# Optimization experiments

Hardware: AMD Instinct MI355X
Metric: run time of the kernel (lower is better)

The kernel has to match this reference:

```python
import jax, jax.numpy as jnp
import numpy as np

DECAY = 0.8
EPS = 1e-05


def setup_inputs() -> dict:
    key = jax.random.key(0)
    k1, k2, k3 = jax.random.split(key, 3)
    x = jax.random.normal(k1, (8, 2048, 256), dtype=jnp.float32)
    embed = jax.random.normal(k2, (8192, 256), dtype=jnp.float32)
    cluster_size = jnp.zeros((8192,), dtype=jnp.float32)
    embed_avg = jax.random.normal(k3, (8192, 256), dtype=jnp.float32)
    return {"x": x, "embed": embed, "cluster_size": cluster_size, "embed_avg": embed_avg}


def reference(x, embed, cluster_size, embed_avg):
    codebook_size, dim = embed.shape
    shape = x.shape
    flatten = x.reshape(-1, dim)  # [N, d]

    dist = -(jnp.sum(flatten ** 2, axis=1, keepdims=True)
             - 2.0 * flatten @ embed.T
             + jnp.sum(embed ** 2, axis=1)[None, :])  # [N, C]
    embed_ind_flat = jnp.argmax(dist, axis=-1)  # [N]
    embed_ind = embed_ind_flat.reshape(shape[:-1])
    quantize = jnp.take(embed, embed_ind_flat, axis=0).reshape(shape)

    # EMA update (training branch). onehot matmuls expressed as segment sums.
    counts = jax.ops.segment_sum(jnp.ones_like(embed_ind_flat, dtype=x.dtype),
                                 embed_ind_flat, num_segments=codebook_size)  # [C]
    embed_sum = jax.ops.segment_sum(flatten, embed_ind_flat,
                                    num_segments=codebook_size)  # [C, d]
    cluster_size_new = cluster_size * DECAY + (1.0 - DECAY) * counts
    embed_avg_new = embed_avg * DECAY + (1.0 - DECAY) * embed_sum
    smoothed = (cluster_size_new + EPS) / (cluster_size_new.sum() + codebook_size * EPS)
    cs = smoothed * cluster_size_new.sum()
    embed_normalized = embed_avg_new / cs[:, None]

    return quantize, embed_ind, embed_normalized, cluster_size_new, embed_avg_new
```

## Files before the change

kernel.cpp:

```cpp
#include <hip/hip_runtime.h>
#include <hip/hip_bf16.h>

#define DECAY_F 0.8f
#define OMD_F   0.2f
#define EPS_F   1e-5f

#define NROWS 16384
#define CBOOK 8192
#define DIM   256
#define KSPLIT 768

#define WS_KEYS   0u
#define WS_ENORM  131072u
#define WS_COUNTS 163840u
#define WS_TOTAL  196608u
#define WS_XSPLIT 262144u
#define WS_ESPLIT_OFF (262144u + 25165824u)
#define WS_NEED   (WS_ESPLIT_OFF + 12582912u)

#define O_QUANT 0
#define O_IND   4194304
#define O_NORM  4210688
#define O_CSN   6307840
#define O_AVG   6316032

typedef __attribute__((ext_vector_type(8))) short short8;
typedef __attribute__((ext_vector_type(4))) float f32x4;
typedef __attribute__((ext_vector_type(4))) unsigned short us4;

__device__ __forceinline__ unsigned int fkey(float f) {
    unsigned int b = __float_as_uint(f);
    return (b & 0x80000000u) ? ~b : (b | 0x80000000u);
}
__device__ __forceinline__ unsigned short f2bf(float f) {
    unsigned int u = __float_as_uint(f);
    unsigned int r = (u + 0x7FFFu + ((u >> 16) & 1u)) >> 16;
    return (unsigned short)r;
}
__device__ __forceinline__ float bf2f(unsigned short h) {
    return __uint_as_float(((unsigned int)h) << 16);
}

#define GLOAD_LDS16(g, l) \
    __builtin_amdgcn_global_load_lds((const __attribute__((address_space(1))) void*)(g), \
                                     (__attribute__((address_space(3))) void*)(l), 16, 0, 0)

__global__ __launch_bounds__(256) void init_avg_kernel(const float* __restrict__ embed_avg,
                                                       float* __restrict__ avg_out) {
    int i = blockIdx.x * 256 + threadIdx.x;
    float4 v = ((const float4*)embed_avg)[i];
    v.x *= DECAY_F; v.y *= DECAY_F; v.z *= DECAY_F; v.w *= DECAY_F;
    ((float4*)avg_out)[i] = v;
}

__global__ __launch_bounds__(256) void xsplit_kernel(const float* __restrict__ src,
                                                     unsigned short* __restrict__ dst) {
    int i = blockIdx.x * 256 + threadIdx.x;
    int e4  = i * 4;
    int row = e4 >> 8;
    int k   = e4 & 255;
    float4 v = ((const float4*)src)[i];
    us4 hi, lo;
    hi.x = f2bf(v.x); lo.x = f2bf(v.x - bf2f(hi.x));
    hi.y = f2bf(v.y); lo.y = f2bf(v.y - bf2f(hi.y));
    hi.z = f2bf(v.z); lo.z = f2bf(v.z - bf2f(hi.z));
    hi.w = f2bf(v.w); lo.w = f2bf(v.w - bf2f(hi.w));
    unsigned short* base = dst + (size_t)row * KSPLIT + k;
    *(us4*)(base + 0)   = hi;
    *(us4*)(base + 256) = lo;
    *(us4*)(base + 512) = hi;
}

__global__ __launch_bounds__(256) void esplit_kernel(const float* __restrict__ embed,
                                                     unsigned short* __restrict__ dst,
                                                     float* __restrict__ enorm) {
    int row  = (blockIdx.x * 256 + threadIdx.x) >> 6;
    int lane = threadIdx.x & 63;
    float4 v = *(const float4*)&embed[row * DIM + lane * 4];
    float s = v.x * v.x + v.y * v.y + v.z * v.z + v.w * v.w;
    for (int m = 32; m >= 1; m >>= 1) s += __shfl_xor(s, m, 64);
    if (lane == 0) enorm[row] = s;
    us4 hi, lo;
    hi.x = f2bf(v.x); lo.x = f2bf(v.x - bf2f(hi.x));
    hi.y = f2bf(v.y); lo.y = f2bf(v.y - bf2f(hi.y));
    hi.z = f2bf(v.z); lo.z = f2bf(v.z - bf2f(hi.z));
    hi.w = f2bf(v.w); lo.w = f2bf(v.w - bf2f(hi.w));
    unsigned short* base = dst + (size_t)row * KSPLIT + lane * 4;
    *(us4*)(base + 0)   = hi;
    *(us4*)(base + 256) = hi;
    *(us4*)(base + 512) = lo;
}

__global__ __launch_bounds__(256, 4) void mfma_argmin_kernel(const unsigned short* __restrict__ A,
                                                             const unsigned short* __restrict__ B,
                                                             const float* __restrict__ enorm,
                                                             unsigned long long* __restrict__ keys) {
    __shared__ __align__(16) unsigned short Al[2][128 * 32];
    __shared__ __align__(16) unsigned short Bl[2][128 * 32];

    const int tid  = threadIdx.x;
    const int lane = tid & 63;
    const int wid  = tid >> 6;
    const int wr = wid >> 1, wc = wid & 1;
    const int mBase = blockIdx.y * 128;
    const int nBase = blockIdx.x * 128;

    const int lr = lane & 15;
    const int hk = lane >> 4;

    f32x4 acc[4][4];
#pragma unroll
    for (int i = 0; i < 4; i++)
#pragma unroll
        for (int n = 0; n < 4; n++) acc[i][n] = (f32x4)0.f;

    const int r0 = tid >> 2;
    const int ck = (((tid & 3) ^ ((r0 >> 1) & 3)) << 3);
    const unsigned short* gA0 = A + (size_t)(mBase + r0) * KSPLIT + ck;
    const unsigned short* gA1 = gA0 + (size_t)64 * KSPLIT;
    const unsigned short* gB0 = B + (size_t)(nBase + r0) * KSPLIT + ck;
    const unsigned short* gB1 = gB0 + (size_t)64 * KSPLIT;

#define STAGE(b, kk) do { \
    GLOAD_LDS16(gA0 + (kk), &Al[b][tid * 8]); \
    GLOAD_LDS16(gA1 + (kk), &Al[b][(tid + 256) * 8]); \
    GLOAD_LDS16(gB0 + (kk), &Bl[b][tid * 8]); \
    GLOAD_LDS16(gB1 + (kk), &Bl[b][(tid + 256) * 8]); \
} while (0)

    const int co = ((hk ^ ((lr >> 1) & 3)) << 3);
    int aoff[4], boff[4];
#pragma unroll
    for (int i = 0; i < 4; i++) {
        aoff[i] = (wr * 64 + i * 16 + lr) * 32 + co;
        boff[i] = (wc * 64 + i * 16 + lr) * 32 + co;
    }

    STAGE(0, 0);
    __syncthreads();

#pragma unroll 2
    for (int t = 0; t < 24; ++t) {
        const int cur = t & 1;
        if (t < 23) STAGE(cur ^ 1, (t + 1) * 32);

        short8 af[4], bf4[4];
#pragma unroll
        for (int i = 0; i < 4; i++) af[i]  = *(const short8*)&Al[cur][aoff[i]];
#pragma unroll
        for (int n = 0; n < 4; n++) bf4[n] = *(const short8*)&Bl[cur][boff[n]];
#pragma unroll
        for (int i = 0; i < 4; i++)
#pragma unroll
            for (int n = 0; n < 4; n++)
                acc[i][n] = __builtin_amdgcn_mfma_f32_16x16x32_bf16(af[i], bf4[n], acc[i][n], 0, 0, 0);

        __syncthreads();
    }
#undef STAGE

    float en4[4];
    int   c4[4];
#pragma unroll
    for (int n = 0; n < 4; n++) {
        c4[n]  = nBase + wc * 64 + n * 16 + lr;
        en4[n] = enorm[c4[n]];
    }
#pragma unroll
    for (int i = 0; i < 4; i++) {
#pragma unroll
        for (int reg = 0; reg < 4; reg++) {
            float bs = 3.4e38f; int bc = 0;
#pragma unroll
            for (int n = 0; n < 4; n++) {
                float s = en4[n] - 2.f * acc[i][n][reg];
                if (s < bs || (s == bs && c4[n] < bc)) { bs = s; bc = c4[n]; }
            }
            unsigned long long key =
                ((unsigned long long)fkey(bs) << 32) | (unsigned int)bc;
#pragma unroll
            for (int m = 8; m >= 1; m >>= 1) {
                unsigned long long o = __shfl_xor(key, m, 64);
                if (o < key) key = o;
            }
            if (lr == 0)
                atomicMin(&keys[mBase + wr * 64 + i * 16 + hk * 4 + reg], key);
        }
    }
}

#define BM 64
#define BN 256
#define KB 16
#define NSPLIT 4

__global__ __launch_bounds__(256) void argmin_kernel(const float* __restrict__ x,
                                                     const float* __restrict__ embed,
                                                     const float* __restrict__ enorm,
                                                     unsigned long long* __restrict__ keys) {
    __shared__ float xs[KB][BM];
    __shared__ float es[KB][BN];

    const int tid = threadIdx.x;
    const int tx = tid & 31;
    const int ty = tid >> 5;
    const int rowBase = blockIdx.x * BM;
    const int cStart = blockIdx.y * (CBOOK / NSPLIT);

    float bestS[8];
    int   bestC[8];
#pragma unroll
    for (int i = 0; i < 8; i++) { bestS[i] = 3.4e38f; bestC[i] = 0; }

    float acc[8][8];

    for (int cb = 0; cb < CBOOK / NSPLIT; cb += BN) {
        const int cbase = cStart + cb;
#pragma unroll
        for (int i = 0; i < 8; i++)
#pragma unroll
            for (int j = 0; j < 8; j++) acc[i][j] = 0.f;

        for (int kk = 0; kk < DIM; kk += KB) {
            __syncthreads();
            {
                int r  = tid >> 2;
                int k4 = (tid & 3) * 4;
                float4 v = *(const float4*)&x[(rowBase + r) * DIM + kk + k4];
                xs[k4 + 0][r] = v.x; xs[k4 + 1][r] = v.y;
                xs[k4 + 2][r] = v.z; xs[k4 + 3][r] = v.w;
            }
            {
                const float4* src = (const float4*)&embed[(cbase + tid) * DIM + kk];
#pragma unroll
                for (int q = 0; q < 4; q++) {
                    float4 v = src[q];
                    es[q * 4 + 0][tid] = v.x; es[q * 4 + 1][tid] = v.y;
                    es[q * 4 + 2][tid] = v.z; es[q * 4 + 3][tid] = v.w;
                }
            }
            __syncthreads();
#pragma unroll
            for (int k = 0; k < KB; k++) {
                float xr[8], er[8];
                *(float4*)&xr[0] = *(const float4*)&xs[k][ty * 8];
                *(float4*)&xr[4] = *(const float4*)&xs[k][ty * 8 + 4];
                *(float4*)&er[0] = *(const float4*)&es[k][tx * 4];
                *(float4*)&er[4] = *(const float4*)&es[k][128 + tx * 4];
#pragma unroll
                for (int i = 0; i < 8; i++)
#pragma unroll
                    for (int j = 0; j < 8; j++)
                        acc[i][j] = fmaf(xr[i], er[j], acc[i][j]);
            }
        }
#pragma unroll
        for (int j = 0; j < 8; j++) {
            int c = cbase + ((j < 4) ? (tx * 4 + j) : (128 + tx * 4 + (j - 4)));
            float en = enorm[c];
#pragma unroll
            for (int i = 0; i < 8; i++) {
                float s = en - 2.f * acc[i][j];
                if (s < bestS[i]) { bestS[i] = s; bestC[i] = c; }
            }
        }
    }

#pragma unroll
    for (int i = 0; i < 8; i++) {
        unsigned long long key =
            ((unsigned long long)fkey(bestS[i]) << 32) | (unsigned int)bestC[i];
        for (int m = 16; m >= 1; m >>= 1) {
            unsigned long long o = __shfl_xor(key, m, 64);
            if (o < key) key = o;
        }
        if (tx == 0) atomicMin(&keys[rowBase + ty * 8 + i], key);
    }
}

__global__ __launch_bounds__(256) void scatter_kernel(const float* __restrict__ x,
                                                      const float* __restrict__ embed,
                                                      const unsigned long long* __restrict__ keys,
                                                      float* __restrict__ quant,
                                                      float* __restrict__ ind_out,
                                                      float* __restrict__ counts,
                                                      float* __restrict__ avg_out) {
    int i = blockIdx.x * 256 + threadIdx.x;
    int row = i >> 6;
    int c4  = (i & 63) * 4;
    int idx = (int)(keys[row] & 0xFFFFFFFFull);
    float4 e = *(const float4*)&embed[idx * DIM + c4];
    *(float4*)&quant[row * DIM + c4] = e;
    float4 xv = *(const float4*)&x[row * DIM + c4];
    atomicAdd(&avg_out[idx * DIM + c4 + 0], OMD_F * xv.x);
    atomicAdd(&avg_out[idx * DIM + c4 + 1], OMD_F * xv.y);
    atomicAdd(&avg_out[idx * DIM + c4 + 2], OMD_F * xv.z);
    atomicAdd(&avg_out[idx * DIM + c4 + 3], OMD_F * xv.w);
    if ((i & 63) == 0) {
        ind_out[row] = (float)idx;
        atomicAdd(&counts[idx], 1.0f);
    }
}

__global__ __launch_bounds__(256) void csn_kernel(const float* __restrict__ cluster_size,
                                                  const float* __restrict__ counts,
                                                  float* __restrict__ csn_out,
                                                  float* __restrict__ total) {
    int c = blockIdx.x * 256 + threadIdx.x;
    float v = DECAY_F * cluster_size[c] + OMD_F * counts[c];
    csn_out[c] = v;
    float s = v;
    for (int m = 32; m >= 1; m >>= 1) s += __shfl_xor(s, m, 64);
    __shared__ float ws4[4];
    if ((threadIdx.x & 63) == 0) ws4[threadIdx.x >> 6] = s;
    __syncthreads();
    if (threadIdx.x == 0) atomicAdd(total, ws4[0] + ws4[1] + ws4[2] + ws4[3]);
}

__global__ __launch_bounds__(256) void norm_kernel(const float* __restrict__ avg_new,
                                                   const float* __restrict__ csn,
                                                   const float* __restrict__ total,
                                                   float* __restrict__ out) {
    int i = blockIdx.x * 256 + threadIdx.x;
    int c = i >> 6;
    float tot = *total;
    float smoothed = (csn[c] + EPS_F) / (tot + (float)CBOOK * EPS_F);
    float cs = smoothed * tot;
    float4 v = ((const float4*)avg_new)[i];
    v.x = v.x / cs; v.y = v.y / cs; v.z = v.z / cs; v.w = v.w / cs;
    ((float4*)out)[i] = v;
}

extern "C" void kernel_launch(void* const* d_in, const int* in_sizes, int n_in,
                              void* d_out, int out_size, void* d_ws, size_t ws_size,
                              hipStream_t stream) {
    const float* x            = (const float*)d_in[0];
    const float* embed        = (const float*)d_in[1];
    const float* cluster_size = (const float*)d_in[2];
    const float* embed_avg    = (const float*)d_in[3];
    float* out = (float*)d_out;
    char*  ws  = (char*)d_ws;

    unsigned long long* keys = (unsigned long long*)(ws + WS_KEYS);
    float* enorm  = (float*)(ws + WS_ENORM);
    float* counts = (float*)(ws + WS_COUNTS);
    float* total  = (float*)(ws + WS_TOTAL);

    hipMemsetAsync(ws + WS_KEYS, 0xFF, NROWS * 8, stream);
    hipMemsetAsync(ws + WS_COUNTS, 0, CBOOK * 4 + 4, stream);

    init_avg_kernel<<<(CBOOK * DIM / 4) / 256, 256, 0, stream>>>(embed_avg, out + O_AVG);

    if (ws_size >= (size_t)WS_NEED) {
        unsigned short* xsplit = (unsigned short*)(ws + WS_XSPLIT);
        unsigned short* esplit = (unsigned short*)(ws + WS_ESPLIT_OFF);
        xsplit_kernel<<<(NROWS * DIM / 4) / 256, 256, 0, stream>>>(x, xsplit);
        esplit_kernel<<<CBOOK / 4, 256, 0, stream>>>(embed, esplit, enorm);
        dim3 grid(CBOOK / 128, NROWS / 128);
        mfma_argmin_kernel<<<grid, 256, 0, stream>>>(xsplit, esplit, enorm, keys);
    } else {
        esplit_kernel<<<CBOOK / 4, 256, 0, stream>>>(embed, (unsigned short*)(ws + WS_XSPLIT), enorm);
        dim3 grid(NROWS / BM, NSPLIT);
        argmin_kernel<<<grid, 256, 0, stream>>>(x, embed, enorm, keys);
    }

    scatter_kernel<<<(NROWS * DIM / 4) / 256, 256, 0, stream>>>(
        x, embed, keys, out + O_QUANT, out + O_IND, counts, out + O_AVG);

    csn_kernel<<<CBOOK / 256, 256, 0, stream>>>(cluster_size, counts, out + O_CSN, total);

    norm_kernel<<<(CBOOK * DIM / 4) / 256, 256, 0, stream>>>(
        out + O_AVG, out + O_CSN, total, out + O_NORM);
}
```

Baseline: 404.8 us.

## Rewrite split-bf16 distance GEMM with 32x32 MFMA, 256x128 tiles, triple buffering

Replaces the 128x128-tile, 16x16x32 MFMA distance kernel with a 256x128 tile using 32x32x16 bf16 MFMA, three-stage LDS buffering with explicit vmcnt waits and a single barrier per step, and a swizzled 1D block order for L2 locality. The larger tile and bigger MFMA shape raise arithmetic intensity and cut LDS reads per flop, and deeper prefetch hides global latency. In exchange, register and LDS use rise (occupancy hint drops to 2 blocks per SIMD set), and the hand-written waitcnt logic must match the number of outstanding loads exactly.

```diff
diff --git a/kernel.cpp b/kernel.cpp
--- a/kernel.cpp
+++ b/kernel.cpp
@@ -24,9 +24,10 @@
 #define O_CSN   6307840
 #define O_AVG   6316032
 
-typedef __attribute__((ext_vector_type(8))) short short8;
-typedef __attribute__((ext_vector_type(4))) float f32x4;
-typedef __attribute__((ext_vector_type(4))) unsigned short us4;
+typedef __attribute__((ext_vector_type(8)))  short short8;
+typedef __attribute__((ext_vector_type(4)))  float f32x4;
+typedef __attribute__((ext_vector_type(16))) float f32x16;
+typedef __attribute__((ext_vector_type(4)))  unsigned short us4;
 
 __device__ __forceinline__ unsigned int fkey(float f) {
     unsigned int b = __float_as_uint(f);
@@ -91,100 +92,138 @@
     *(us4*)(base + 512) = lo;
 }
 
-__global__ __launch_bounds__(256, 4) void mfma_argmin_kernel(const unsigned short* __restrict__ A,
-                                                             const unsigned short* __restrict__ B,
-                                                             const float* __restrict__ enorm,
-                                                             unsigned long long* __restrict__ keys) {
-    __shared__ __align__(16) unsigned short Al[2][128 * 32];
-    __shared__ __align__(16) unsigned short Bl[2][128 * 32];
+__global__ __launch_bounds__(256, 2) void mfma32_argmin_kernel(
+        const unsigned short* __restrict__ A,
+        const unsigned short* __restrict__ B,
+        const float* __restrict__ enorm,
+        unsigned long long* __restrict__ keys) {
+    __shared__ __align__(16) unsigned short Al[3][8192];
+    __shared__ __align__(16) unsigned short Bl[3][4096];
 
     const int tid  = threadIdx.x;
     const int lane = tid & 63;
     const int wid  = tid >> 6;
-    const int wr = wid >> 1, wc = wid & 1;
-    const int mBase = blockIdx.y * 128;
-    const int nBase = blockIdx.x * 128;
-
-    const int lr = lane & 15;
-    const int hk = lane >> 4;
-
-    f32x4 acc[4][4];
-#pragma unroll
-    for (int i = 0; i < 4; i++)
-#pragma unroll
-        for (int n = 0; n < 4; n++) acc[i][n] = (f32x4)0.f;
-
-    const int r0 = tid >> 2;
-    const int ck = (((tid & 3) ^ ((r0 >> 1) & 3)) << 3);
-    const unsigned short* gA0 = A + (size_t)(mBase + r0) * KSPLIT + ck;
-    const unsigned short* gA1 = gA0 + (size_t)64 * KSPLIT;
-    const unsigned short* gB0 = B + (size_t)(nBase + r0) * KSPLIT + ck;
-    const unsigned short* gB1 = gB0 + (size_t)64 * KSPLIT;
-
-#define STAGE(b, kk) do { \
-    GLOAD_LDS16(gA0 + (kk), &Al[b][tid * 8]); \
-    GLOAD_LDS16(gA1 + (kk), &Al[b][(tid + 256) * 8]); \
-    GLOAD_LDS16(gB0 + (kk), &Bl[b][tid * 8]); \
-    GLOAD_LDS16(gB1 + (kk), &Bl[b][(tid + 256) * 8]); \
+    const int wr   = wid >> 1;
+    const int wc   = wid & 1;
+    const int l31  = lane & 31;
+    const int hi5  = lane >> 5;
+
+    const int bid  = blockIdx.x;
+    const int swz  = ((bid & 7) << 9) | (bid >> 3);
+    const int stid = swz >> 6, win = swz & 63;
+    const int by   = ((stid >> 3) << 3) + (win >> 3);
+    const int bx   = ((stid & 7) << 3) + (win & 7);
+    const int mBase = by << 8;
+    const int nBase = bx << 7;
+
+    f32x16 acc[4][2];
+#pragma unroll
+    for (int m = 0; m < 4; m++)
+#pragma unroll
+        for (int n = 0; n < 2; n++) acc[m][n] = (f32x16)0.f;
+
+    const unsigned short* pA[4];
+    int dA[4];
+#pragma unroll
+    for (int c = 0; c < 4; c++) {
+        int slot = (wid * 4 + c) * 64 + lane;
+        int row  = slot >> 2;
+        int lg   = (slot & 3) ^ (row & 3);
+        pA[c] = A + (size_t)(mBase + row) * KSPLIT + lg * 8;
+        dA[c] = slot * 8;
+    }
+    const unsigned short* pB[2];
+    int dB[2];
+#pragma unroll
+    for (int c = 0; c < 2; c++) {
+        int slot = (wid * 2 + c) * 64 + lane;
+        int row  = slot >> 2;
+        int lg   = (slot & 3) ^ (row & 3);
+        pB[c] = B + (size_t)(nBase + row) * KSPLIT + lg * 8;
+        dB[c] = slot * 8;
+    }
+
+#define STAGE(bufn, t) do { \
+    _Pragma("unroll") for (int c = 0; c < 4; c++) \
+        GLOAD_LDS16(pA[c] + (t) * 32, &Al[bufn][dA[c]]); \
+    _Pragma("unroll") for (int c = 0; c < 2; c++) \
+        GLOAD_LDS16(pB[c] + (t) * 32, &Bl[bufn][dB[c]]); \
 } while (0)
 
-    const int co = ((hk ^ ((lr >> 1) & 3)) << 3);
-    int aoff[4], boff[4];
-#pragma unroll
-    for (int i = 0; i < 4; i++) {
-        aoff[i] = (wr * 64 + i * 16 + lr) * 32 + co;
-        boff[i] = (wc * 64 + i * 16 + lr) * 32 + co;
-    }
+    const int cx = l31 & 3;
+    const int co0 = ((0 * 2 + hi5) ^ cx) * 8;
+    const int co1 = ((1 * 2 + hi5) ^ cx) * 8;
+    int arow[4], brow[2];
+#pragma unroll
+    for (int m = 0; m < 4; m++) arow[m] = (wr * 128 + m * 32 + l31) * 32;
+#pragma unroll
+    for (int n = 0; n < 2; n++) brow[n] = (wc * 64 + n * 32 + l31) * 32;
 
     STAGE(0, 0);
-    __syncthreads();
-
-#pragma unroll 2
+    STAGE(1, 1);
+
+    int b0 = 0, b1 = 1, b2 = 2;
     for (int t = 0; t < 24; ++t) {
-        const int cur = t & 1;
-        if (t < 23) STAGE(cur ^ 1, (t + 1) * 32);
-
-        short8 af[4], bf4[4];
-#pragma unroll
-        for (int i = 0; i < 4; i++) af[i]  = *(const short8*)&Al[cur][aoff[i]];
-#pragma unroll
-        for (int n = 0; n < 4; n++) bf4[n] = *(const short8*)&Bl[cur][boff[n]];
-#pragma unroll
-        for (int i = 0; i < 4; i++)
-#pragma unroll
-            for (int n = 0; n < 4; n++)
-                acc[i][n] = __builtin_amdgcn_mfma_f32_16x16x32_bf16(af[i], bf4[n], acc[i][n], 0, 0, 0);
-
-        __syncthreads();
+        if (t < 23) asm volatile("s_waitcnt vmcnt(6)" ::: "memory");
+        else        asm volatile("s_waitcnt vmcnt(0)" ::: "memory");
+        asm volatile("s_barrier" ::: "memory");
+        if (t < 22) STAGE(b2, t + 2);
+
+        short8 af[4][2], bf[2][2];
+#pragma unroll
+        for (int m = 0; m < 4; m++) {
+            af[m][0] = *(const short8*)&Al[b0][arow[m] + co0];
+            af[m][1] = *(const short8*)&Al[b0][arow[m] + co1];
+        }
+#pragma unroll
+        for (int n = 0; n < 2; n++) {
+            bf[n][0] = *(const short8*)&Bl[b0][brow[n] + co0];
+            bf[n][1] = *(const short8*)&Bl[b0][brow[n] + co1];
+        }
+        asm volatile("s_waitcnt lgkmcnt(0)" ::: "memory");
+        __builtin_amdgcn_sched_barrier(0);
+        __builtin_amdgcn_s_setprio(1);
+#pragma unroll
+        for (int m = 0; m < 4; m++)
+#pragma unroll
+            for (int n = 0; n < 2; n++) {
+                acc[m][n] = __builtin_amdgcn_mfma_f32_32x32x16_bf16(
+                    af[m][0], bf[n][0], acc[m][n], 0, 0, 0);
+                acc[m][n] = __builtin_amdgcn_mfma_f32_32x32x16_bf16(
+                    af[m][1], bf[n][1], acc[m][n], 0, 0, 0);
+            }
+        __builtin_amdgcn_s_setprio(0);
+
+        int nb0 = b1; b1 = b2; b2 = b0; b0 = nb0;
     }
 #undef STAGE
 
-    float en4[4];
-    int   c4[4];
-#pragma unroll
-    for (int n = 0; n < 4; n++) {
-        c4[n]  = nBase + wc * 64 + n * 16 + lr;
-        en4[n] = enorm[c4[n]];
-    }
-#pragma unroll
-    for (int i = 0; i < 4; i++) {
-#pragma unroll
-        for (int reg = 0; reg < 4; reg++) {
-            float bs = 3.4e38f; int bc = 0;
-#pragma unroll
-            for (int n = 0; n < 4; n++) {
-                float s = en4[n] - 2.f * acc[i][n][reg];
-                if (s < bs || (s == bs && c4[n] < bc)) { bs = s; bc = c4[n]; }
-            }
+    float en[2];
+    int   cc[2];
+#pragma unroll
+    for (int n = 0; n < 2; n++) {
+        cc[n] = nBase + wc * 64 + n * 32 + l31;
+        en[n] = enorm[cc[n]];
+    }
+#pragma unroll
+    for (int m = 0; m < 4; m++) {
+#pragma unroll
+        for (int r = 0; r < 16; r++) {
+            float s0 = en[0] - 2.f * acc[m][0][r];
+            float s1 = en[1] - 2.f * acc[m][1][r];
+            float bs = s0; int bc = cc[0];
+            if (s1 < bs) { bs = s1; bc = cc[1]; }
             unsigned long long key =
                 ((unsigned long long)fkey(bs) << 32) | (unsigned int)bc;
 #pragma unroll
-            for (int m = 8; m >= 1; m >>= 1) {
-                unsigned long long o = __shfl_xor(key, m, 64);
+            for (int msk = 16; msk >= 1; msk >>= 1) {
+                unsigned long long o = __shfl_xor(key, msk, 64);
                 if (o < key) key = o;
             }
-            if (lr == 0)
-                atomicMin(&keys[mBase + wr * 64 + i * 16 + hk * 4 + reg], key);
+            if (l31 == 0) {
+                int grow = mBase + wr * 128 + m * 32 + (r & 3) + 8 * (r >> 2) + 4 * hi5;
+                atomicMin(&keys[grow], key);
+            }
         }
     }
 }
@@ -356,8 +395,8 @@
         unsigned short* esplit = (unsigned short*)(ws + WS_ESPLIT_OFF);
         xsplit_kernel<<<(NROWS * DIM / 4) / 256, 256, 0, stream>>>(x, xsplit);
         esplit_kernel<<<CBOOK / 4, 256, 0, stream>>>(embed, esplit, enorm);
-        dim3 grid(CBOOK / 128, NROWS / 128);
-        mfma_argmin_kernel<<<grid, 256, 0, stream>>>(xsplit, esplit, enorm, keys);
+        mfma32_argmin_kernel<<<(NROWS / 256) * (CBOOK / 128), 256, 0, stream>>>(
+            xsplit, esplit, enorm, keys);
     } else {
         esplit_kernel<<<CBOOK / 4, 256, 0, stream>>>(embed, (unsigned short*)(ws + WS_XSPLIT), enorm);
         dim3 grid(NROWS / BM, NSPLIT);
```

New measurement: 512.2 us. 26.5% more time.

## Use 256x256 tiles with 8 waves and triple-buffered pipelined MFMA argmin

Applied to the files above, without the earlier changes.

Replaces the 128x128, 4-wave, double-buffered bf16-split MFMA distance kernel with a 256x256 tile, 8-wave kernel. It uses a three-stage LDS ring with split A/B prefetch interleaved between two MFMA half-phases, explicit waitcnt/barrier control, and s_setprio around the MFMA bursts. It also applies an XCD-aware block swizzle to the 1D grid. The aims are higher arithmetic intensity per loaded byte and better overlap of global-to-LDS loads with MFMA work. The cost is one block per CU, larger LDS use and accumulator register pressure, and fragile hand-written synchronisation.

```diff
diff --git a/kernel.cpp b/kernel.cpp
--- a/kernel.cpp
+++ b/kernel.cpp
@@ -24,9 +24,9 @@
 #define O_CSN   6307840
 #define O_AVG   6316032
 
-typedef __attribute__((ext_vector_type(8))) short short8;
-typedef __attribute__((ext_vector_type(4))) float f32x4;
-typedef __attribute__((ext_vector_type(4))) unsigned short us4;
+typedef __attribute__((ext_vector_type(8)))  short short8;
+typedef __attribute__((ext_vector_type(4)))  float f32x4;
+typedef __attribute__((ext_vector_type(4)))  unsigned short us4;
 
 __device__ __forceinline__ unsigned int fkey(float f) {
     unsigned int b = __float_as_uint(f);
@@ -91,100 +91,142 @@
     *(us4*)(base + 512) = lo;
 }
 
-__global__ __launch_bounds__(256, 4) void mfma_argmin_kernel(const unsigned short* __restrict__ A,
-                                                             const unsigned short* __restrict__ B,
-                                                             const float* __restrict__ enorm,
-                                                             unsigned long long* __restrict__ keys) {
-    __shared__ __align__(16) unsigned short Al[2][128 * 32];
-    __shared__ __align__(16) unsigned short Bl[2][128 * 32];
+__global__ __launch_bounds__(512, 1) void mfma8_argmin_kernel(
+        const unsigned short* __restrict__ A,
+        const unsigned short* __restrict__ B,
+        const float* __restrict__ enorm,
+        unsigned long long* __restrict__ keys) {
+    __shared__ __align__(16) unsigned short Al[3][8192];
+    __shared__ __align__(16) unsigned short Bl[3][8192];
 
     const int tid  = threadIdx.x;
     const int lane = tid & 63;
     const int wid  = tid >> 6;
-    const int wr = wid >> 1, wc = wid & 1;
-    const int mBase = blockIdx.y * 128;
-    const int nBase = blockIdx.x * 128;
-
-    const int lr = lane & 15;
-    const int hk = lane >> 4;
-
-    f32x4 acc[4][4];
-#pragma unroll
-    for (int i = 0; i < 4; i++)
-#pragma unroll
-        for (int n = 0; n < 4; n++) acc[i][n] = (f32x4)0.f;
-
-    const int r0 = tid >> 2;
-    const int ck = (((tid & 3) ^ ((r0 >> 1) & 3)) << 3);
-    const unsigned short* gA0 = A + (size_t)(mBase + r0) * KSPLIT + ck;
-    const unsigned short* gA1 = gA0 + (size_t)64 * KSPLIT;
-    const unsigned short* gB0 = B + (size_t)(nBase + r0) * KSPLIT + ck;
-    const unsigned short* gB1 = gB0 + (size_t)64 * KSPLIT;
-
-#define STAGE(b, kk) do { \
-    GLOAD_LDS16(gA0 + (kk), &Al[b][tid * 8]); \
-    GLOAD_LDS16(gA1 + (kk), &Al[b][(tid + 256) * 8]); \
-    GLOAD_LDS16(gB0 + (kk), &Bl[b][tid * 8]); \
-    GLOAD_LDS16(gB1 + (kk), &Bl[b][(tid + 256) * 8]); \
+    const int wr   = wid >> 2;
+    const int wc   = wid & 3;
+    const int lr   = lane & 15;
+    const int hk   = lane >> 4;
+
+    const int bid = blockIdx.x;
+    const int swz = ((bid & 7) << 8) | (bid >> 3);
+    const int bx  = swz & 31;
+    const int by  = swz >> 5;
+    const int mBase = by << 8;
+    const int nBase = bx << 8;
+
+    f32x4 acc[8][4];
+#pragma unroll
+    for (int m = 0; m < 8; m++)
+#pragma unroll
+        for (int n = 0; n < 4; n++) acc[m][n] = (f32x4)0.f;
+
+    const unsigned short* gA[2]; int ldA[2];
+    const unsigned short* gB[2]; int ldB[2];
+#pragma unroll
+    for (int l = 0; l < 2; l++) {
+        int slot = l * 512 + tid;
+        int row  = slot >> 2;
+        int lg   = (slot & 3) ^ ((row >> 1) & 3);
+        gA[l] = A + (size_t)(mBase + row) * KSPLIT + lg * 8;
+        ldA[l] = slot * 8;
+        gB[l] = B + (size_t)(nBase + row) * KSPLIT + lg * 8;
+        ldB[l] = slot * 8;
+    }
+
+#define STAGE_A(bufn, t) do { \
+    GLOAD_LDS16(gA[0] + (t) * 32, &Al[bufn][ldA[0]]); \
+    GLOAD_LDS16(gA[1] + (t) * 32, &Al[bufn][ldA[1]]); \
 } while (0)
-
-    const int co = ((hk ^ ((lr >> 1) & 3)) << 3);
-    int aoff[4], boff[4];
-#pragma unroll
-    for (int i = 0; i < 4; i++) {
-        aoff[i] = (wr * 64 + i * 16 + lr) * 32 + co;
-        boff[i] = (wc * 64 + i * 16 + lr) * 32 + co;
-    }
-
-    STAGE(0, 0);
-    __syncthreads();
-
-#pragma unroll 2
+#define STAGE_B(bufn, t) do { \
+    GLOAD_LDS16(gB[0] + (t) * 32, &Bl[bufn][ldB[0]]); \
+    GLOAD_LDS16(gB[1] + (t) * 32, &Bl[bufn][ldB[1]]); \
+} while (0)
+
+    const int co = (hk ^ ((lr >> 1) & 3)) << 3;
+    int aoff[8], boff[4];
+#pragma unroll
+    for (int m = 0; m < 8; m++) aoff[m] = (wr * 128 + m * 16 + lr) * 32 + co;
+#pragma unroll
+    for (int n = 0; n < 4; n++) boff[n] = (wc * 64 + n * 16 + lr) * 32 + co;
+
+    STAGE_A(0, 0); STAGE_B(0, 0);
+    STAGE_A(1, 1); STAGE_B(1, 1);
+    asm volatile("s_waitcnt vmcnt(4)" ::: "memory");
+    asm volatile("s_barrier" ::: "memory");
+
+    int buf = 0, nbuf = 2;
     for (int t = 0; t < 24; ++t) {
-        const int cur = t & 1;
-        if (t < 23) STAGE(cur ^ 1, (t + 1) * 32);
-
-        short8 af[4], bf4[4];
-#pragma unroll
-        for (int i = 0; i < 4; i++) af[i]  = *(const short8*)&Al[cur][aoff[i]];
-#pragma unroll
-        for (int n = 0; n < 4; n++) bf4[n] = *(const short8*)&Bl[cur][boff[n]];
-#pragma unroll
-        for (int i = 0; i < 4; i++)
+        const unsigned short* ab = &Al[buf][0];
+        const unsigned short* bb = &Bl[buf][0];
+        short8 av[4], bv[4];
+
+#pragma unroll
+        for (int m = 0; m < 4; m++) av[m] = *(const short8*)&ab[aoff[m]];
+#pragma unroll
+        for (int n = 0; n < 4; n++) bv[n] = *(const short8*)&bb[boff[n]];
+        if (t < 22) STAGE_A(nbuf, t + 2);
+        asm volatile("s_barrier" ::: "memory");
+        asm volatile("s_waitcnt lgkmcnt(0)" ::: "memory");
+        __builtin_amdgcn_sched_barrier(0);
+        __builtin_amdgcn_s_setprio(1);
+#pragma unroll
+        for (int m = 0; m < 4; m++)
 #pragma unroll
             for (int n = 0; n < 4; n++)
-                acc[i][n] = __builtin_amdgcn_mfma_f32_16x16x32_bf16(af[i], bf4[n], acc[i][n], 0, 0, 0);
-
-        __syncthreads();
-    }
-#undef STAGE
-
-    float en4[4];
-    int   c4[4];
+                acc[m][n] = __builtin_amdgcn_mfma_f32_16x16x32_bf16(av[m], bv[n], acc[m][n], 0, 0, 0);
+        __builtin_amdgcn_s_setprio(0);
+        asm volatile("s_barrier" ::: "memory");
+
+#pragma unroll
+        for (int m = 0; m < 4; m++) av[m] = *(const short8*)&ab[aoff[4 + m]];
+        if (t < 22) STAGE_B(nbuf, t + 2);
+        asm volatile("s_barrier" ::: "memory");
+        asm volatile("s_waitcnt lgkmcnt(0)" ::: "memory");
+        __builtin_amdgcn_sched_barrier(0);
+        __builtin_amdgcn_s_setprio(1);
+#pragma unroll
+        for (int m = 0; m < 4; m++)
+#pragma unroll
+            for (int n = 0; n < 4; n++)
+                acc[4 + m][n] = __builtin_amdgcn_mfma_f32_16x16x32_bf16(av[m], bv[n], acc[4 + m][n], 0, 0, 0);
+        __builtin_amdgcn_s_setprio(0);
+        if (t < 22)      asm volatile("s_waitcnt vmcnt(4)" ::: "memory");
+        else if (t < 23) asm volatile("s_waitcnt vmcnt(0)" ::: "memory");
+        asm volatile("s_barrier" ::: "memory");
+
+        int nb = buf + 1; if (nb == 3) nb = 0;
+        int nn = nbuf + 1; if (nn == 3) nn = 0;
+        buf = nb; nbuf = nn;
+    }
+#undef STAGE_A
+#undef STAGE_B
+
+    float en[4];
+    int   cc[4];
 #pragma unroll
     for (int n = 0; n < 4; n++) {
-        c4[n]  = nBase + wc * 64 + n * 16 + lr;
-        en4[n] = enorm[c4[n]];
-    }
-#pragma unroll
-    for (int i = 0; i < 4; i++) {
+        cc[n] = nBase + wc * 64 + n * 16 + lr;
+        en[n] = enorm[cc[n]];
+    }
+#pragma unroll
+    for (int m = 0; m < 8; m++) {
 #pragma unroll
         for (int reg = 0; reg < 4; reg++) {
             float bs = 3.4e38f; int bc = 0;
 #pragma unroll
             for (int n = 0; n < 4; n++) {
-                float s = en4[n] - 2.f * acc[i][n][reg];
-                if (s < bs || (s == bs && c4[n] < bc)) { bs = s; bc = c4[n]; }
+                float s = en[n] - 2.f * acc[m][n][reg];
+                if (s < bs || (s == bs && cc[n] < bc)) { bs = s; bc = cc[n]; }
             }
             unsigned long long key =
                 ((unsigned long long)fkey(bs) << 32) | (unsigned int)bc;
 #pragma unroll
-            for (int m = 8; m >= 1; m >>= 1) {
-                unsigned long long o = __shfl_xor(key, m, 64);
+            for (int msk = 8; msk >= 1; msk >>= 1) {
+                unsigned long long o = __shfl_xor(key, msk, 64);
                 if (o < key) key = o;
             }
             if (lr == 0)
-                atomicMin(&keys[mBase + wr * 64 + i * 16 + hk * 4 + reg], key);
+                atomicMin(&keys[mBase + wr * 128 + m * 16 + hk * 4 + reg], key);
         }
     }
 }
@@ -356,8 +398,8 @@
         unsigned short* esplit = (unsigned short*)(ws + WS_ESPLIT_OFF);
         xsplit_kernel<<<(NROWS * DIM / 4) / 256, 256, 0, stream>>>(x, xsplit);
         esplit_kernel<<<CBOOK / 4, 256, 0, stream>>>(embed, esplit, enorm);
-        dim3 grid(CBOOK / 128, NROWS / 128);
-        mfma_argmin_kernel<<<grid, 256, 0, stream>>>(xsplit, esplit, enorm, keys);
+        mfma8_argmin_kernel<<<(NROWS / 256) * (CBOOK / 256), 512, 0, stream>>>(
+            xsplit, esplit, enorm, keys);
     } else {
         esplit_kernel<<<CBOOK / 4, 256, 0, stream>>>(embed, (unsigned short*)(ws + WS_XSPLIT), enorm);
         dim3 grid(NROWS / BM, NSPLIT);
```

Result: slower. 631.3 us (+55.9%).
